# Performance work log

Hardware: AMD Instinct MI355X
Metric: run time of the kernel (lower is better)

Reference implementation:

```python
import jax, jax.numpy as jnp
import numpy as np

B, S, D, H = 2, 2048, 1024, 16
HD = D // H  # 64


def setup_inputs() -> dict:
    key = jax.random.key(0)
    ks = jax.random.split(key, 7)
    std = 1.0 / np.sqrt(D)
    return {
        "q": jax.random.normal(ks[0], (B, S, D), jnp.float32),
        "k": jax.random.normal(ks[1], (B, S, D), jnp.float32),
        "v": jax.random.normal(ks[2], (B, S, D), jnp.float32),
        "w_q": jax.random.normal(ks[3], (D, D), jnp.float32) * std,
        "w_k": jax.random.normal(ks[4], (D, D), jnp.float32) * std,
        "w_v": jax.random.normal(ks[5], (D, D), jnp.float32) * std,
        "w_o": jax.random.normal(ks[6], (D, D), jnp.float32) * std,
    }


def reference(q, k, v, w_q, w_k, w_v, w_o):
    # Linear (torch nn.Linear, no bias): y = x @ W.T
    Q = jnp.einsum('bsd,ed->bse', q, w_q)
    K = jnp.einsum('bsd,ed->bse', k, w_k)
    V = jnp.einsum('bsd,ed->bse', v, w_v)
    # split heads -> (B, H, S, HD)
    Qh = Q.reshape(B, S, H, HD).transpose(0, 2, 1, 3)
    Kh = K.reshape(B, S, H, HD).transpose(0, 2, 1, 3)
    Vh = V.reshape(B, S, H, HD).transpose(0, 2, 1, 3)
    scale = 1.0 / np.sqrt(HD).astype(np.float32)
    scores = jnp.einsum('bhqd,bhkd->bhqk', Qh, Kh) * scale  # [B,H,S,S]
    attn = jax.nn.softmax(scores, axis=-1)
    ctx = jnp.einsum('bhqk,bhkd->bhqd', attn, Vh)
    combined = ctx.transpose(0, 2, 1, 3).reshape(B, S, D)
    out = jnp.einsum('bsd,ed->bse', combined, w_o)
    return out, attn
```

## Files before the change

kernel.cpp:

```cpp
#include <hip/hip_runtime.h>
#include <hip/hip_bf16.h>
#include <cstdint>

#define B_ 2
#define S_ 2048
#define D_ 1024
#define H_ 16
#define HD_ 64

#define SCALE_LOG2 0.18033688011112042f

typedef __attribute__((ext_vector_type(8))) __bf16 bf16x8;
typedef __attribute__((ext_vector_type(8))) unsigned short ushort8;
typedef __attribute__((ext_vector_type(4))) unsigned short ushort4v;
typedef __attribute__((ext_vector_type(4))) float f32x4;

__device__ __forceinline__ unsigned short f2bf(float f) {
  __bf16 h = (__bf16)f;
  return __builtin_bit_cast(unsigned short, h);
}

__device__ __forceinline__ float bf2f(unsigned short u) {
  union { unsigned int i; float f; } v; v.i = ((unsigned int)u) << 16; return v.f;
}

__device__ __forceinline__ float fexp2(float x) {
#if __has_builtin(__builtin_amdgcn_exp2f)
  return __builtin_amdgcn_exp2f(x);
#else
  return exp2f(x);
#endif
}

__device__ __forceinline__ f32x4 mfma16(bf16x8 a, bf16x8 b, f32x4 c) {
  return __builtin_amdgcn_mfma_f32_16x16x32_bf16(a, b, c, 0, 0, 0);
}

#define LGKM_BARRIER()                                        \
  do {                                                        \
    asm volatile("s_waitcnt lgkmcnt(0)" ::: "memory");        \
    __builtin_amdgcn_s_barrier();                             \
  } while (0)

#define SWZ(r, sc) ((sc) ^ (((r) & 3) << 4))

__global__ __launch_bounds__(256) void proj_qkv_kernel(
    const float* __restrict__ qin, const float* __restrict__ kin,
    const float* __restrict__ vin, const float* __restrict__ wq,
    const float* __restrict__ wk, const float* __restrict__ wv,
    unsigned short* __restrict__ qh, unsigned short* __restrict__ kh,
    unsigned short* __restrict__ vt)
{
  __shared__ unsigned short As[128][40];
  __shared__ unsigned short Bs[128][40];

  const int z = blockIdx.z;
  const float* X = (z == 0) ? qin : (z == 1) ? kin : vin;
  const float* W = (z == 0) ? wq : (z == 1) ? wk : wv;
  unsigned short* dst = (z == 0) ? qh : (z == 1) ? kh : vt;
  const float osc = (z == 0) ? SCALE_LOG2 : 1.0f;

  const int lin = blockIdx.x + 8 * blockIdx.y;
  const int swz = (lin & 7) * 32 + (lin >> 3);
  const int bx = swz & 7, by = swz >> 3;

  const int tid = threadIdx.x;
  const int lane = tid & 63, wid = tid >> 6;
  const int c = lane & 15, g = lane >> 4;
  const int wr = wid >> 1, wc = wid & 1;
  const int m0 = by * 128, n0 = bx * 128;

  const int sr = tid >> 1, sh = tid & 1;
  const float* Ap = X + (size_t)(m0 + sr) * D_ + sh * 16;
  const float* Bp = W + (size_t)(n0 + sr) * D_ + sh * 16;

  float ar[16], br[16];
  f32x4 acc[4][4];
#pragma unroll
  for (int i = 0; i < 4; ++i)
#pragma unroll
    for (int j = 0; j < 4; ++j) acc[i][j] = (f32x4){0.f, 0.f, 0.f, 0.f};

  auto ldg_tile = [&](int kt) {
    const float* ap = Ap + kt * 32;
    const float* bp = Bp + kt * 32;
#pragma unroll
    for (int j = 0; j < 4; ++j) {
      *(f32x4*)(ar + 4 * j) = *(const f32x4*)(ap + 4 * j);
      *(f32x4*)(br + 4 * j) = *(const f32x4*)(bp + 4 * j);
    }
  };
  auto sts_tile = [&]() {
    unsigned short ta[16], tb[16];
#pragma unroll
    for (int j = 0; j < 16; ++j) { ta[j] = f2bf(ar[j]); tb[j] = f2bf(br[j]); }
    *(ushort8*)&As[sr][sh * 16]     = *(ushort8*)&ta[0];
    *(ushort8*)&As[sr][sh * 16 + 8] = *(ushort8*)&ta[8];
    *(ushort8*)&Bs[sr][sh * 16]     = *(ushort8*)&tb[0];
    *(ushort8*)&Bs[sr][sh * 16 + 8] = *(ushort8*)&tb[8];
  };

  ldg_tile(0);
  sts_tile();
  __syncthreads();

  for (int kt = 0; kt < 32; ++kt) {
    if (kt < 31) ldg_tile(kt + 1);
    bf16x8 af[4], bfr[4];
#pragma unroll
    for (int i = 0; i < 4; ++i) af[i]  = *(bf16x8*)&As[wr * 64 + i * 16 + c][g * 8];
#pragma unroll
    for (int i = 0; i < 4; ++i) bfr[i] = *(bf16x8*)&Bs[wc * 64 + i * 16 + c][g * 8];
#pragma unroll
    for (int mi = 0; mi < 4; ++mi)
#pragma unroll
      for (int ni = 0; ni < 4; ++ni)
        acc[mi][ni] = mfma16(af[mi], bfr[ni], acc[mi][ni]);
    __syncthreads();
    if (kt < 31) { sts_tile(); __syncthreads(); }
  }

#pragma unroll
  for (int mi = 0; mi < 4; ++mi) {
#pragma unroll
    for (int ni = 0; ni < 4; ++ni) {
      const int n = n0 + wc * 64 + ni * 16 + c;
      const int h = n >> 6, hd = n & 63;
      if (z < 2) {
#pragma unroll
        for (int r = 0; r < 4; ++r) {
          const int m = m0 + wr * 64 + mi * 16 + g * 4 + r;
          const int b = m >> 11, s = m & 2047;
          dst[((size_t)(b * H_ + h) * S_ + s) * HD_ + hd] = f2bf(acc[mi][ni][r] * osc);
        }
      } else {
        const int m = m0 + wr * 64 + mi * 16 + g * 4;
        const int b = m >> 11, s = m & 2047;
        ushort4v pk;
#pragma unroll
        for (int r = 0; r < 4; ++r) pk[r] = f2bf(acc[mi][ni][r]);
        *(ushort4v*)&dst[((size_t)(b * H_ + h) * HD_ + hd) * S_ + s] = pk;
      }
    }
  }
}

__global__ __launch_bounds__(256) void attn_kernel(
    const unsigned short* __restrict__ qh, const unsigned short* __restrict__ kh,
    const unsigned short* __restrict__ vt, float* __restrict__ attn,
    unsigned short* __restrict__ comb)
{
  __shared__ unsigned short Ks[64][64];
  __shared__ unsigned short Vs[64][64];
  __shared__ unsigned short Ps[4][16][88];

  const int tid = threadIdx.x;
  const int lane = tid & 63, w = tid >> 6;
  const int c = lane & 15, g = lane >> 4;

  const int lin = blockIdx.x;
  const int swz = (lin & 7) * 64 + (lin >> 3);
  const int bh = swz >> 4;
  const int q0 = (swz & 15) * 128;

  const unsigned short* Qb = qh + (size_t)bh * S_ * HD_;
  const unsigned short* Kb = kh + (size_t)bh * S_ * HD_;
  const unsigned short* Vb = vt + (size_t)bh * HD_ * S_;
  float* attnb = attn + (size_t)bh * S_ * S_;

  const int sr = tid >> 2;
  const int scol = (tid & 3) * 16;
  const int swcol = SWZ(sr, scol);

  bf16x8 aQA[2], aQB[2];
#pragma unroll
  for (int t = 0; t < 2; ++t) {
    aQA[t] = *(const bf16x8*)(Qb + (size_t)(q0 + w * 16 + c) * HD_ + t * 32 + g * 8);
    aQB[t] = *(const bf16x8*)(Qb + (size_t)(q0 + 64 + w * 16 + c) * HD_ + t * 32 + g * 8);
  }

  const unsigned short* Kst = Kb + (size_t)sr * HD_ + scol;
  const unsigned short* Vst = Vb + (size_t)sr * S_ + scol;

  float lA = 0.f, lB = 0.f;
  {
    ushort8 kr0 = *(const ushort8*)Kst;
    ushort8 kr1 = *(const ushort8*)(Kst + 8);
    for (int kt = 0; kt < 32; ++kt) {
      *(ushort8*)&Ks[sr][swcol]     = kr0;
      *(ushort8*)&Ks[sr][swcol + 8] = kr1;
      LGKM_BARRIER();
      if (kt < 31) {
        const unsigned short* p = Kst + (size_t)(kt + 1) * 64 * HD_;
        kr0 = *(const ushort8*)p;
        kr1 = *(const ushort8*)(p + 8);
      }
#pragma unroll
      for (int ni = 0; ni < 4; ++ni) {
        bf16x8 k0 = *(bf16x8*)&Ks[ni * 16 + c][SWZ(c, g * 8)];
        bf16x8 k1 = *(bf16x8*)&Ks[ni * 16 + c][SWZ(c, 32 + g * 8)];
        f32x4 a = (f32x4){0.f, 0.f, 0.f, 0.f};
        a = mfma16(k0, aQA[0], a);
        a = mfma16(k1, aQA[1], a);
        lA += (fexp2(a[0]) + fexp2(a[1])) + (fexp2(a[2]) + fexp2(a[3]));
      }
      LGKM_BARRIER();
    }
  }
  lA += __shfl_xor(lA, 16);
  lA += __shfl_xor(lA, 32);
  const float invlA = 1.f / lA;

  f32x4 ctxA[4], ctxB[4];
#pragma unroll
  for (int ni = 0; ni < 4; ++ni) {
    ctxA[ni] = (f32x4){0.f, 0.f, 0.f, 0.f};
    ctxB[ni] = (f32x4){0.f, 0.f, 0.f, 0.f};
  }

  unsigned short* psrow = &Ps[w][c][g * 4];
  float* srowA = attnb + (size_t)(q0 + w * 16 + g) * S_ + c * 4;
  float* srowB = attnb + (size_t)(q0 + 64 + w * 16 + g) * S_ + c * 4;

  {
    ushort8 kr0 = *(const ushort8*)Kst;
    ushort8 kr1 = *(const ushort8*)(Kst + 8);
    ushort8 vr0 = *(const ushort8*)Vst;
    ushort8 vr1 = *(const ushort8*)(Vst + 8);

    for (int kt = 0; kt < 32; ++kt) {
      *(ushort8*)&Ks[sr][swcol]     = kr0;
      *(ushort8*)&Ks[sr][swcol + 8] = kr1;
      *(ushort8*)&Vs[sr][swcol]     = vr0;
      *(ushort8*)&Vs[sr][swcol + 8] = vr1;
      LGKM_BARRIER();
      if (kt < 31) {
        const unsigned short* p = Kst + (size_t)(kt + 1) * 64 * HD_;
        const unsigned short* q = Vst + (kt + 1) * 64;
        kr0 = *(const ushort8*)p;
        kr1 = *(const ushort8*)(p + 8);
        vr0 = *(const ushort8*)q;
        vr1 = *(const ushort8*)(q + 8);
      }

#pragma unroll
      for (int ni = 0; ni < 4; ++ni) {
        bf16x8 k0 = *(bf16x8*)&Ks[ni * 16 + c][SWZ(c, g * 8)];
        bf16x8 k1 = *(bf16x8*)&Ks[ni * 16 + c][SWZ(c, 32 + g * 8)];
        f32x4 a = (f32x4){0.f, 0.f, 0.f, 0.f};
        a = mfma16(k0, aQA[0], a);
        a = mfma16(k1, aQA[1], a);
        ushort4v pk;
#pragma unroll
        for (int r = 0; r < 4; ++r) pk[r] = f2bf(fexp2(a[r]) * invlA);
        *(ushort4v*)(psrow + ni * 16) = pk;
        f32x4 b = (f32x4){0.f, 0.f, 0.f, 0.f};
        b = mfma16(k0, aQB[0], b);
        b = mfma16(k1, aQB[1], b);
        lB += (fexp2(b[0]) + fexp2(b[1])) + (fexp2(b[2]) + fexp2(b[3]));
      }

      bf16x8 aP[2];
#pragma unroll
      for (int t = 0; t < 2; ++t) aP[t] = *(bf16x8*)&Ps[w][c][t * 32 + g * 8];
#pragma unroll
      for (int ni = 0; ni < 4; ++ni)
#pragma unroll
        for (int t = 0; t < 2; ++t)
          ctxA[ni] = mfma16(aP[t],
                            *(bf16x8*)&Vs[ni * 16 + c][SWZ(c, t * 32 + g * 8)],
                            ctxA[ni]);

#pragma unroll
      for (int it = 0; it < 4; ++it) {
        ushort4v pb = *(ushort4v*)&Ps[w][it * 4 + g][c * 4];
        f32x4 pf;
#pragma unroll
        for (int r = 0; r < 4; ++r) pf[r] = bf2f(pb[r]);
        __builtin_nontemporal_store(pf, (f32x4*)(srowA + (size_t)it * 4 * S_ + kt * 64));
      }
      LGKM_BARRIER();
    }
  }
  lB += __shfl_xor(lB, 16);
  lB += __shfl_xor(lB, 32);
  const float invlB = 1.f / lB;

  {
    ushort8 kr0 = *(const ushort8*)Kst;
    ushort8 kr1 = *(const ushort8*)(Kst + 8);
    ushort8 vr0 = *(const ushort8*)Vst;
    ushort8 vr1 = *(const ushort8*)(Vst + 8);

    for (int kt = 0; kt < 32; ++kt) {
      *(ushort8*)&Ks[sr][swcol]     = kr0;
      *(ushort8*)&Ks[sr][swcol + 8] = kr1;
      *(ushort8*)&Vs[sr][swcol]     = vr0;
      *(ushort8*)&Vs[sr][swcol + 8] = vr1;
      LGKM_BARRIER();
      if (kt < 31) {
        const unsigned short* p = Kst + (size_t)(kt + 1) * 64 * HD_;
        const unsigned short* q = Vst + (kt + 1) * 64;
        kr0 = *(const ushort8*)p;
        kr1 = *(const ushort8*)(p + 8);
        vr0 = *(const ushort8*)q;
        vr1 = *(const ushort8*)(q + 8);
      }

#pragma unroll
      for (int ni = 0; ni < 4; ++ni) {
        bf16x8 k0 = *(bf16x8*)&Ks[ni * 16 + c][SWZ(c, g * 8)];
        bf16x8 k1 = *(bf16x8*)&Ks[ni * 16 + c][SWZ(c, 32 + g * 8)];
        f32x4 b = (f32x4){0.f, 0.f, 0.f, 0.f};
        b = mfma16(k0, aQB[0], b);
        b = mfma16(k1, aQB[1], b);
        ushort4v pk;
#pragma unroll
        for (int r = 0; r < 4; ++r) pk[r] = f2bf(fexp2(b[r]) * invlB);
        *(ushort4v*)(psrow + ni * 16) = pk;
      }

      bf16x8 aP[2];
#pragma unroll
      for (int t = 0; t < 2; ++t) aP[t] = *(bf16x8*)&Ps[w][c][t * 32 + g * 8];
#pragma unroll
      for (int ni = 0; ni < 4; ++ni)
#pragma unroll
        for (int t = 0; t < 2; ++t)
          ctxB[ni] = mfma16(aP[t],
                            *(bf16x8*)&Vs[ni * 16 + c][SWZ(c, t * 32 + g * 8)],
                            ctxB[ni]);

#pragma unroll
      for (int it = 0; it < 4; ++it) {
        ushort4v pb = *(ushort4v*)&Ps[w][it * 4 + g][c * 4];
        f32x4 pf;
#pragma unroll
        for (int r = 0; r < 4; ++r) pf[r] = bf2f(pb[r]);
        __builtin_nontemporal_store(pf, (f32x4*)(srowB + (size_t)it * 4 * S_ + kt * 64));
      }
      LGKM_BARRIER();
    }
  }

  const int b = bh >> 4, h = bh & 15;
#pragma unroll
  for (int ni = 0; ni < 4; ++ni)
#pragma unroll
    for (int r = 0; r < 4; ++r) {
      comb[(size_t)(b * S_ + q0 + w * 16 + g * 4 + r) * D_ + h * 64 + ni * 16 + c] =
          f2bf(ctxA[ni][r]);
      comb[(size_t)(b * S_ + q0 + 64 + w * 16 + g * 4 + r) * D_ + h * 64 + ni * 16 + c] =
          f2bf(ctxB[ni][r]);
    }
}

__global__ __launch_bounds__(256) void out_proj_kernel(
    const unsigned short* __restrict__ comb, const float* __restrict__ wo,
    float* __restrict__ out)
{
  __shared__ unsigned short As[128][40];
  __shared__ unsigned short Bs[128][40];

  const int lin = blockIdx.x + 8 * blockIdx.y;
  const int swz = (lin & 7) * 32 + (lin >> 3);
  const int bx = swz & 7, by = swz >> 3;

  const int tid = threadIdx.x;
  const int lane = tid & 63, wid = tid >> 6;
  const int c = lane & 15, g = lane >> 4;
  const int wr = wid >> 1, wc = wid & 1;
  const int m0 = by * 128, n0 = bx * 128;
  const int sr = tid >> 1, sh = tid & 1;

  const unsigned short* Apb = comb + (size_t)(m0 + sr) * D_ + sh * 16;
  const float* Bpb = wo + (size_t)(n0 + sr) * D_ + sh * 16;

  ushort8 ar2[2];
  float br[16];
  f32x4 acc[4][4];
#pragma unroll
  for (int i = 0; i < 4; ++i)
#pragma unroll
    for (int j = 0; j < 4; ++j) acc[i][j] = (f32x4){0.f, 0.f, 0.f, 0.f};

  auto ldg_tile = [&](int kt) {
    ar2[0] = *(const ushort8*)(Apb + kt * 32);
    ar2[1] = *(const ushort8*)(Apb + kt * 32 + 8);
#pragma unroll
    for (int j = 0; j < 4; ++j)
      *(f32x4*)(br + 4 * j) = *(const f32x4*)(Bpb + kt * 32 + 4 * j);
  };
  auto sts_tile = [&]() {
    *(ushort8*)&As[sr][sh * 16]     = ar2[0];
    *(ushort8*)&As[sr][sh * 16 + 8] = ar2[1];
    unsigned short tb[16];
#pragma unroll
    for (int j = 0; j < 16; ++j) tb[j] = f2bf(br[j]);
    *(ushort8*)&Bs[sr][sh * 16]     = *(ushort8*)&tb[0];
    *(ushort8*)&Bs[sr][sh * 16 + 8] = *(ushort8*)&tb[8];
  };

  ldg_tile(0);
  sts_tile();
  __syncthreads();

  for (int kt = 0; kt < 32; ++kt) {
    if (kt < 31) ldg_tile(kt + 1);
    bf16x8 af[4], bfr[4];
#pragma unroll
    for (int i = 0; i < 4; ++i) af[i]  = *(bf16x8*)&As[wr * 64 + i * 16 + c][g * 8];
#pragma unroll
    for (int i = 0; i < 4; ++i) bfr[i] = *(bf16x8*)&Bs[wc * 64 + i * 16 + c][g * 8];
#pragma unroll
    for (int mi = 0; mi < 4; ++mi)
#pragma unroll
      for (int ni = 0; ni < 4; ++ni)
        acc[mi][ni] = mfma16(af[mi], bfr[ni], acc[mi][ni]);
    __syncthreads();
    if (kt < 31) { sts_tile(); __syncthreads(); }
  }

#pragma unroll
  for (int mi = 0; mi < 4; ++mi)
#pragma unroll
    for (int ni = 0; ni < 4; ++ni)
#pragma unroll
      for (int r = 0; r < 4; ++r) {
        const int m = m0 + wr * 64 + mi * 16 + g * 4 + r;
        const int n = n0 + wc * 64 + ni * 16 + c;
        out[(size_t)m * D_ + n] = acc[mi][ni][r];
      }
}

extern "C" void kernel_launch(void* const* d_in, const int* in_sizes, int n_in,
                              void* d_out, int out_size, void* d_ws, size_t ws_size,
                              hipStream_t stream)
{
  const float* q  = (const float*)d_in[0];
  const float* k  = (const float*)d_in[1];
  const float* v  = (const float*)d_in[2];
  const float* wq = (const float*)d_in[3];
  const float* wk = (const float*)d_in[4];
  const float* wv = (const float*)d_in[5];
  const float* wo = (const float*)d_in[6];

  float* out  = (float*)d_out;
  float* attn = out + (size_t)B_ * S_ * D_;

  const size_t NE = (size_t)B_ * S_ * D_;
  unsigned short* qh   = (unsigned short*)d_ws;
  unsigned short* kh   = qh + NE;
  unsigned short* vt   = kh + NE;
  unsigned short* comb = vt + NE;

  proj_qkv_kernel<<<dim3(8, 32, 3), dim3(256), 0, stream>>>(q, k, v, wq, wk, wv, qh, kh, vt);
  attn_kernel<<<dim3(512), dim3(256), 0, stream>>>(qh, kh, vt, attn, comb);
  out_proj_kernel<<<dim3(8, 32), dim3(256), 0, stream>>>(comb, wo, out);
}
```

Before: 227.0 us.

## Pre-cast inputs to bf16 and use direct global-to-LDS loads in GEMMs

Adds a cast kernel that converts activations and weights to bf16 once, folding the softmax scale into w_q. The bf16 copies go into the attn output buffer as scratch and into the workspace. Both projection GEMMs then load tiles straight into LDS with global_load_lds, read through an XOR swizzle, and drop the register-staged fp32 conversion path. In exchange there is an extra launch and an extra round trip to memory for the casts, and the GEMM loop loses its register prefetch overlap: each iteration issues its load and then waits at a barrier.

```diff
diff --git a/kernel.cpp b/kernel.cpp
--- a/kernel.cpp
+++ b/kernel.cpp
@@ -36,6 +36,12 @@
   return __builtin_amdgcn_mfma_f32_16x16x32_bf16(a, b, c, 0, 0, 0);
 }
 
+__device__ __forceinline__ void gload16(const unsigned short* g, unsigned short* l) {
+  __builtin_amdgcn_global_load_lds(
+      (const __attribute__((address_space(1))) unsigned int*)g,
+      (__attribute__((address_space(3))) unsigned int*)l, 16, 0, 0);
+}
+
 #define LGKM_BARRIER()                                        \
   do {                                                        \
     asm volatile("s_waitcnt lgkmcnt(0)" ::: "memory");        \
@@ -44,80 +50,103 @@
 
 #define SWZ(r, sc) ((sc) ^ (((r) & 3) << 4))
 
+__global__ __launch_bounds__(256) void cast_kernel(
+    const float* __restrict__ q, const float* __restrict__ k,
+    const float* __restrict__ v, const float* __restrict__ wq,
+    const float* __restrict__ wk, const float* __restrict__ wv,
+    const float* __restrict__ wo,
+    unsigned short* __restrict__ xq, unsigned short* __restrict__ xk,
+    unsigned short* __restrict__ xv, unsigned short* __restrict__ wqb,
+    unsigned short* __restrict__ wkb, unsigned short* __restrict__ wvb,
+    unsigned short* __restrict__ wob)
+{
+  const size_t M4 = (size_t)4 << 20, M1 = (size_t)1 << 20;
+  size_t i = ((size_t)blockIdx.x * 256 + threadIdx.x) * 8;
+  const float* src; unsigned short* dst; float sc = 1.f; size_t off;
+  if (i < M4)                 { src = q;  dst = xq;  off = i; }
+  else if (i < 2 * M4)        { src = k;  dst = xk;  off = i - M4; }
+  else if (i < 3 * M4)        { src = v;  dst = xv;  off = i - 2 * M4; }
+  else if (i < 3 * M4 + M1)   { src = wq; dst = wqb; off = i - 3 * M4; sc = SCALE_LOG2; }
+  else if (i < 3 * M4 + 2*M1) { src = wk; dst = wkb; off = i - 3 * M4 - M1; }
+  else if (i < 3 * M4 + 3*M1) { src = wv; dst = wvb; off = i - 3 * M4 - 2 * M1; }
+  else                        { src = wo; dst = wob; off = i - 3 * M4 - 3 * M1; }
+  f32x4 a = *(const f32x4*)(src + off);
+  f32x4 b = *(const f32x4*)(src + off + 4);
+  ushort8 o;
+#pragma unroll
+  for (int r = 0; r < 4; ++r) { o[r] = f2bf(a[r] * sc); o[4 + r] = f2bf(b[r] * sc); }
+  *(ushort8*)(dst + off) = o;
+}
+
 __global__ __launch_bounds__(256) void proj_qkv_kernel(
-    const float* __restrict__ qin, const float* __restrict__ kin,
-    const float* __restrict__ vin, const float* __restrict__ wq,
-    const float* __restrict__ wk, const float* __restrict__ wv,
+    const unsigned short* __restrict__ xq, const unsigned short* __restrict__ xk,
+    const unsigned short* __restrict__ xv, const unsigned short* __restrict__ wqb,
+    const unsigned short* __restrict__ wkb, const unsigned short* __restrict__ wvb,
     unsigned short* __restrict__ qh, unsigned short* __restrict__ kh,
     unsigned short* __restrict__ vt)
 {
-  __shared__ unsigned short As[128][40];
-  __shared__ unsigned short Bs[128][40];
+  __shared__ unsigned short As[128 * 32];
+  __shared__ unsigned short Bs[128 * 32];
 
   const int z = blockIdx.z;
-  const float* X = (z == 0) ? qin : (z == 1) ? kin : vin;
-  const float* W = (z == 0) ? wq : (z == 1) ? wk : wv;
+  const unsigned short* X = (z == 0) ? xq : (z == 1) ? xk : xv;
+  const unsigned short* W = (z == 0) ? wqb : (z == 1) ? wkb : wvb;
   unsigned short* dst = (z == 0) ? qh : (z == 1) ? kh : vt;
-  const float osc = (z == 0) ? SCALE_LOG2 : 1.0f;
 
   const int lin = blockIdx.x + 8 * blockIdx.y;
   const int swz = (lin & 7) * 32 + (lin >> 3);
   const int bx = swz & 7, by = swz >> 3;
 
   const int tid = threadIdx.x;
-  const int lane = tid & 63, wid = tid >> 6;
+  const int lane = tid & 63, w = tid >> 6;
   const int c = lane & 15, g = lane >> 4;
-  const int wr = wid >> 1, wc = wid & 1;
+  const int wr = w >> 1, wc = w & 1;
   const int m0 = by * 128, n0 = bx * 128;
 
-  const int sr = tid >> 1, sh = tid & 1;
-  const float* Ap = X + (size_t)(m0 + sr) * D_ + sh * 16;
-  const float* Bp = W + (size_t)(n0 + sr) * D_ + sh * 16;
-
-  float ar[16], br[16];
+  const int arow = 2 * w * 16 + (lane >> 2);
+  const int cs = (lane & 3) ^ ((lane >> 2) & 3);
+  const unsigned short* Asrc0 = X + (size_t)(m0 + arow) * D_ + cs * 8;
+  const unsigned short* Asrc1 = Asrc0 + (size_t)16 * D_;
+  const unsigned short* Bsrc0 = W + (size_t)(n0 + arow) * D_ + cs * 8;
+  const unsigned short* Bsrc1 = Bsrc0 + (size_t)16 * D_;
+  unsigned short* Adst0 = &As[(2 * w) * 16 * 32];
+  unsigned short* Adst1 = &As[(2 * w + 1) * 16 * 32];
+  unsigned short* Bdst0 = &Bs[(2 * w) * 16 * 32];
+  unsigned short* Bdst1 = &Bs[(2 * w + 1) * 16 * 32];
+
   f32x4 acc[4][4];
 #pragma unroll
   for (int i = 0; i < 4; ++i)
 #pragma unroll
     for (int j = 0; j < 4; ++j) acc[i][j] = (f32x4){0.f, 0.f, 0.f, 0.f};
 
-  auto ldg_tile = [&](int kt) {
-    const float* ap = Ap + kt * 32;
-    const float* bp = Bp + kt * 32;
-#pragma unroll
-    for (int j = 0; j < 4; ++j) {
-      *(f32x4*)(ar + 4 * j) = *(const f32x4*)(ap + 4 * j);
-      *(f32x4*)(br + 4 * j) = *(const f32x4*)(bp + 4 * j);
-    }
-  };
-  auto sts_tile = [&]() {
-    unsigned short ta[16], tb[16];
-#pragma unroll
-    for (int j = 0; j < 16; ++j) { ta[j] = f2bf(ar[j]); tb[j] = f2bf(br[j]); }
-    *(ushort8*)&As[sr][sh * 16]     = *(ushort8*)&ta[0];
-    *(ushort8*)&As[sr][sh * 16 + 8] = *(ushort8*)&ta[8];
-    *(ushort8*)&Bs[sr][sh * 16]     = *(ushort8*)&tb[0];
-    *(ushort8*)&Bs[sr][sh * 16 + 8] = *(ushort8*)&tb[8];
-  };
-
-  ldg_tile(0);
-  sts_tile();
-  __syncthreads();
+  const int rslot = 8 * 0;
+  (void)rslot;
 
   for (int kt = 0; kt < 32; ++kt) {
-    if (kt < 31) ldg_tile(kt + 1);
+    gload16(Asrc0 + kt * 32, Adst0);
+    gload16(Asrc1 + kt * 32, Adst1);
+    gload16(Bsrc0 + kt * 32, Bdst0);
+    gload16(Bsrc1 + kt * 32, Bdst1);
+    __syncthreads();
+
     bf16x8 af[4], bfr[4];
 #pragma unroll
-    for (int i = 0; i < 4; ++i) af[i]  = *(bf16x8*)&As[wr * 64 + i * 16 + c][g * 8];
-#pragma unroll
-    for (int i = 0; i < 4; ++i) bfr[i] = *(bf16x8*)&Bs[wc * 64 + i * 16 + c][g * 8];
+    for (int i = 0; i < 4; ++i) {
+      const int row = wr * 64 + i * 16 + c;
+      af[i] = *(bf16x8*)&As[row * 32 + 8 * (g ^ (c & 3))];
+    }
+#pragma unroll
+    for (int i = 0; i < 4; ++i) {
+      const int row = wc * 64 + i * 16 + c;
+      bfr[i] = *(bf16x8*)&Bs[row * 32 + 8 * (g ^ (c & 3))];
+    }
 #pragma unroll
     for (int mi = 0; mi < 4; ++mi)
 #pragma unroll
       for (int ni = 0; ni < 4; ++ni)
         acc[mi][ni] = mfma16(af[mi], bfr[ni], acc[mi][ni]);
     __syncthreads();
-    if (kt < 31) { sts_tile(); __syncthreads(); }
   }
 
 #pragma unroll
@@ -131,7 +160,7 @@
         for (int r = 0; r < 4; ++r) {
           const int m = m0 + wr * 64 + mi * 16 + g * 4 + r;
           const int b = m >> 11, s = m & 2047;
-          dst[((size_t)(b * H_ + h) * S_ + s) * HD_ + hd] = f2bf(acc[mi][ni][r] * osc);
+          dst[((size_t)(b * H_ + h) * S_ + s) * HD_ + hd] = f2bf(acc[mi][ni][r]);
         }
       } else {
         const int m = m0 + wr * 64 + mi * 16 + g * 4;
@@ -356,69 +385,63 @@
 }
 
 __global__ __launch_bounds__(256) void out_proj_kernel(
-    const unsigned short* __restrict__ comb, const float* __restrict__ wo,
+    const unsigned short* __restrict__ comb, const unsigned short* __restrict__ wob,
     float* __restrict__ out)
 {
-  __shared__ unsigned short As[128][40];
-  __shared__ unsigned short Bs[128][40];
+  __shared__ unsigned short As[128 * 32];
+  __shared__ unsigned short Bs[128 * 32];
 
   const int lin = blockIdx.x + 8 * blockIdx.y;
   const int swz = (lin & 7) * 32 + (lin >> 3);
   const int bx = swz & 7, by = swz >> 3;
 
   const int tid = threadIdx.x;
-  const int lane = tid & 63, wid = tid >> 6;
+  const int lane = tid & 63, w = tid >> 6;
   const int c = lane & 15, g = lane >> 4;
-  const int wr = wid >> 1, wc = wid & 1;
+  const int wr = w >> 1, wc = w & 1;
   const int m0 = by * 128, n0 = bx * 128;
-  const int sr = tid >> 1, sh = tid & 1;
-
-  const unsigned short* Apb = comb + (size_t)(m0 + sr) * D_ + sh * 16;
-  const float* Bpb = wo + (size_t)(n0 + sr) * D_ + sh * 16;
-
-  ushort8 ar2[2];
-  float br[16];
+
+  const int arow = 2 * w * 16 + (lane >> 2);
+  const int cs = (lane & 3) ^ ((lane >> 2) & 3);
+  const unsigned short* Asrc0 = comb + (size_t)(m0 + arow) * D_ + cs * 8;
+  const unsigned short* Asrc1 = Asrc0 + (size_t)16 * D_;
+  const unsigned short* Bsrc0 = wob + (size_t)(n0 + arow) * D_ + cs * 8;
+  const unsigned short* Bsrc1 = Bsrc0 + (size_t)16 * D_;
+  unsigned short* Adst0 = &As[(2 * w) * 16 * 32];
+  unsigned short* Adst1 = &As[(2 * w + 1) * 16 * 32];
+  unsigned short* Bdst0 = &Bs[(2 * w) * 16 * 32];
+  unsigned short* Bdst1 = &Bs[(2 * w + 1) * 16 * 32];
+
   f32x4 acc[4][4];
 #pragma unroll
   for (int i = 0; i < 4; ++i)
 #pragma unroll
     for (int j = 0; j < 4; ++j) acc[i][j] = (f32x4){0.f, 0.f, 0.f, 0.f};
 
-  auto ldg_tile = [&](int kt) {
-    ar2[0] = *(const ushort8*)(Apb + kt * 32);
-    ar2[1] = *(const ushort8*)(Apb + kt * 32 + 8);
-#pragma unroll
-    for (int j = 0; j < 4; ++j)
-      *(f32x4*)(br + 4 * j) = *(const f32x4*)(Bpb + kt * 32 + 4 * j);
-  };
-  auto sts_tile = [&]() {
-    *(ushort8*)&As[sr][sh * 16]     = ar2[0];
-    *(ushort8*)&As[sr][sh * 16 + 8] = ar2[1];
-    unsigned short tb[16];
-#pragma unroll
-    for (int j = 0; j < 16; ++j) tb[j] = f2bf(br[j]);
-    *(ushort8*)&Bs[sr][sh * 16]     = *(ushort8*)&tb[0];
-    *(ushort8*)&Bs[sr][sh * 16 + 8] = *(ushort8*)&tb[8];
-  };
-
-  ldg_tile(0);
-  sts_tile();
-  __syncthreads();
-
   for (int kt = 0; kt < 32; ++kt) {
-    if (kt < 31) ldg_tile(kt + 1);
+    gload16(Asrc0 + kt * 32, Adst0);
+    gload16(Asrc1 + kt * 32, Adst1);
+    gload16(Bsrc0 + kt * 32, Bdst0);
+    gload16(Bsrc1 + kt * 32, Bdst1);
+    __syncthreads();
+
     bf16x8 af[4], bfr[4];
 #pragma unroll
-    for (int i = 0; i < 4; ++i) af[i]  = *(bf16x8*)&As[wr * 64 + i * 16 + c][g * 8];
-#pragma unroll
-    for (int i = 0; i < 4; ++i) bfr[i] = *(bf16x8*)&Bs[wc * 64 + i * 16 + c][g * 8];
+    for (int i = 0; i < 4; ++i) {
+      const int row = wr * 64 + i * 16 + c;
+      af[i] = *(bf16x8*)&As[row * 32 + 8 * (g ^ (c & 3))];
+    }
+#pragma unroll
+    for (int i = 0; i < 4; ++i) {
+      const int row = wc * 64 + i * 16 + c;
+      bfr[i] = *(bf16x8*)&Bs[row * 32 + 8 * (g ^ (c & 3))];
+    }
 #pragma unroll
     for (int mi = 0; mi < 4; ++mi)
 #pragma unroll
       for (int ni = 0; ni < 4; ++ni)
         acc[mi][ni] = mfma16(af[mi], bfr[ni], acc[mi][ni]);
     __syncthreads();
-    if (kt < 31) { sts_tile(); __syncthreads(); }
   }
 
 #pragma unroll
@@ -449,12 +472,26 @@
   float* attn = out + (size_t)B_ * S_ * D_;
 
   const size_t NE = (size_t)B_ * S_ * D_;
+  const size_t M1 = (size_t)D_ * D_;
+
+  unsigned short* scr = (unsigned short*)attn;
+  unsigned short* xq  = scr;
+  unsigned short* xk  = xq + NE;
+  unsigned short* xv  = xk + NE;
+  unsigned short* wqb = xv + NE;
+  unsigned short* wkb = wqb + M1;
+  unsigned short* wvb = wkb + M1;
+
   unsigned short* qh   = (unsigned short*)d_ws;
   unsigned short* kh   = qh + NE;
   unsigned short* vt   = kh + NE;
   unsigned short* comb = vt + NE;
-
-  proj_qkv_kernel<<<dim3(8, 32, 3), dim3(256), 0, stream>>>(q, k, v, wq, wk, wv, qh, kh, vt);
+  unsigned short* wob  = comb + NE;
+
+  cast_kernel<<<dim3(8192), dim3(256), 0, stream>>>(
+      q, k, v, wq, wk, wv, wo, xq, xk, xv, wqb, wkb, wvb, wob);
+  proj_qkv_kernel<<<dim3(8, 32, 3), dim3(256), 0, stream>>>(
+      xq, xk, xv, wqb, wkb, wvb, qh, kh, vt);
   attn_kernel<<<dim3(512), dim3(256), 0, stream>>>(qh, kh, vt, attn, comb);
-  out_proj_kernel<<<dim3(8, 32), dim3(256), 0, stream>>>(comb, wo, out);
-}
+  out_proj_kernel<<<dim3(8, 32), dim3(256), 0, stream>>>(comb, wob, out);
+}
```

After: 209.3 us. 1.08x faster.
